# Kernel tuning notes

Measured on AMD Instinct MI355X. Metric: run time of the kernel, lower is better.

Reference implementation:

```python
import jax, jax.numpy as jnp
import numpy as np

D_STATE = 16
D_CONV = 4
DT_RANK = 8


def layer_norm(x, g, b, eps=1e-5):
    m = x.mean(-1, keepdims=True)
    v = ((x - m) ** 2).mean(-1, keepdims=True)
    return (x - m) / jnp.sqrt(v + eps) * g + b


def rms_norm(x, w, eps=1e-5):
    return x * jax.lax.rsqrt(jnp.mean(x * x, -1, keepdims=True) + eps) * w


def mamba_layer(feat, in_proj_w, conv_w, conv_b, x_proj_w, dt_proj_w, dt_proj_b,
                A_log, D_param, out_proj_w, rms_w):
    # feat: [N, C] treated as a length-N sequence with batch 1 (residual block)
    x_in = rms_norm(feat, rms_w)
    xz = x_in @ in_proj_w                         # [N, 2*d_inner]
    d_inner = conv_w.shape[0]
    x, z = xz[:, :d_inner], xz[:, d_inner:]
    # causal depthwise conv1d (torch pad=d_conv-1 then truncate to L)
    L = x.shape[0]
    x_pad = jnp.pad(x, ((D_CONV - 1, 0), (0, 0)))
    xc = conv_b + sum(x_pad[k:k + L, :] * conv_w[:, k] for k in range(D_CONV))
    x = jax.nn.silu(xc)
    dbc = x @ x_proj_w                            # [N, dt_rank + 2*d_state]
    delta = jax.nn.softplus(dbc[:, :DT_RANK] @ dt_proj_w + dt_proj_b)  # [N, d_inner]
    Bm = dbc[:, DT_RANK:DT_RANK + D_STATE]        # [N, d_state]
    Cm = dbc[:, DT_RANK + D_STATE:]               # [N, d_state]
    A = -jnp.exp(A_log)                           # [d_inner, d_state]

    def step(h, inp):
        d_t, b_t, c_t, x_t = inp
        dA = jnp.exp(d_t[:, None] * A)            # [d_inner, d_state]
        h = dA * h + d_t[:, None] * b_t[None, :] * x_t[:, None]
        y_t = (h * c_t[None, :]).sum(-1)          # [d_inner]
        return h, y_t

    h0 = jnp.zeros((d_inner, D_STATE), feat.dtype)
    _, y = jax.lax.scan(step, h0, (delta, Bm, Cm, x))
    y = y + D_param * x
    y = y * jax.nn.silu(z)
    return feat + y @ out_proj_w                  # residual


def setup_inputs() -> dict:
    N, K, C = 32768, 16, 128
    d_inner = 2 * C
    key = jax.random.key(0)
    ks = jax.random.split(key, 12)
    s = 0.02
    inp = {
        "feat": jax.random.normal(ks[0], (N, C), jnp.float32),
        "coord": jax.random.normal(ks[1], (N, 3), jnp.float32),
        "reference_index": jax.random.randint(ks[2], (N, K), 0, N, jnp.int32),
        "gauss_dist": jax.random.uniform(ks[3], (N, K), jnp.float32),
        "j": 0,
        # Mamba params
        "in_proj_w": jax.random.normal(ks[4], (C, 2 * d_inner), jnp.float32) * s,
        "conv_w": jax.random.normal(ks[5], (d_inner, D_CONV), jnp.float32) * s,
        "conv_b": jnp.zeros((d_inner,), jnp.float32),
        "x_proj_w": jax.random.normal(ks[6], (d_inner, DT_RANK + 2 * D_STATE), jnp.float32) * s,
        "dt_proj_w": jax.random.normal(ks[7], (DT_RANK, d_inner), jnp.float32) * s,
        "dt_proj_b": jax.random.uniform(ks[8], (d_inner,), jnp.float32) * 0.1,
        "A_log": jnp.log(jnp.tile(jnp.arange(1.0, D_STATE + 1.0, dtype=jnp.float32), (d_inner, 1))),
        "D_param": jnp.ones((d_inner,), jnp.float32),
        "out_proj_w": jax.random.normal(ks[9], (d_inner, C), jnp.float32) * s,
        "rms_w": jnp.ones((C,), jnp.float32),
        # PointBatchNorm (LayerNorm) shared for both norms
        "ln_g": jnp.ones((C,), jnp.float32),
        "ln_b": jnp.zeros((C,), jnp.float32),
        # linear_attention: Linear(2C->C), LayerNorm, ReLU, Linear(C->C)
        "la_w1": jax.random.normal(ks[10], (2 * C, C), jnp.float32) * s,
        "la_b1": jnp.zeros((C,), jnp.float32),
        "la_ln_g": jnp.ones((C,), jnp.float32),
        "la_ln_b": jnp.zeros((C,), jnp.float32),
        "la_w2": jax.random.normal(ks[11], (C, C), jnp.float32) * s,
        "la_b2": jnp.zeros((C,), jnp.float32),
    }
    return inp


def reference(feat, coord, reference_index, gauss_dist, j,
              in_proj_w, conv_w, conv_b, x_proj_w, dt_proj_w, dt_proj_b,
              A_log, D_param, out_proj_w, rms_w, ln_g, ln_b,
              la_w1, la_b1, la_ln_g, la_ln_b, la_w2, la_b2):
    # pointops.grouping(with_xyz=False): gather neighbor features [N, K, C]
    group_feat = feat[reference_index]
    combined = (gauss_dist[..., None] * group_feat).sum(axis=1)     # [N, C]
    combined = layer_norm(combined, ln_g, ln_b)
    feat_mamba = mamba_layer(feat, in_proj_w, conv_w, conv_b, x_proj_w,
                             dt_proj_w, dt_proj_b, A_log, D_param,
                             out_proj_w, rms_w)
    feat_mamba = layer_norm(feat_mamba, ln_g, ln_b)
    cat_feat = jnp.concatenate([feat_mamba, combined], axis=-1)     # [N, 2C]
    h = jax.nn.relu(layer_norm(cat_feat @ la_w1 + la_b1, la_ln_g, la_ln_b))
    return h @ la_w2 + la_b2
```

## Files before the change

kernel.cpp:

```cpp
#include <hip/hip_runtime.h>
#include <hip/hip_bf16.h>
#include <math.h>

#define N_TOK 32768
#define LC 32
#define NCHUNK (N_TOK / LC)
#define NSEG 64
#define SEGLEN (NCHUNK / NSEG)
#define MIDROWS 67
#define XPAD 264

typedef short short8 __attribute__((ext_vector_type(8)));
typedef float f32x4 __attribute__((ext_vector_type(4)));

__device__ __forceinline__ float siluf_(float v){ return v / (1.f + __expf(-v)); }
__device__ __forceinline__ float softplusf_(float v){ return v > 20.f ? v : log1pf(__expf(v)); }

__device__ __forceinline__ unsigned f2bfu(float f){
  __hip_bfloat16 h = __float2bfloat16(f);
  return (unsigned)*(unsigned short*)&h;
}
__device__ __forceinline__ float bfu2f(unsigned short u){
  __hip_bfloat16 h; *(unsigned short*)&h = u; return __bfloat162float(h);
}

__device__ __forceinline__ float waveRed64(float v){
  #pragma unroll
  for (int m = 1; m < 64; m <<= 1) v += __shfl_xor(v, m);
  return v;
}

__device__ __forceinline__ void pow_chain(float w, float pw[16]){
  pw[0]=w; pw[1]=w*w; pw[2]=pw[1]*w; pw[3]=pw[1]*pw[1];
  pw[4]=pw[3]*pw[0]; pw[5]=pw[3]*pw[1]; pw[6]=pw[3]*pw[2]; pw[7]=pw[3]*pw[3];
  pw[8]=pw[7]*pw[0]; pw[9]=pw[7]*pw[1]; pw[10]=pw[7]*pw[2]; pw[11]=pw[7]*pw[3];
  pw[12]=pw[7]*pw[4]; pw[13]=pw[7]*pw[5]; pw[14]=pw[7]*pw[6]; pw[15]=pw[7]*pw[7];
}

__device__ __forceinline__ bool check_intA(const float aS[16]){
  bool ok = true;
  #pragma unroll
  for (int s=0;s<16;s++){
    float tgt = (float)(s+1);
    if (fabsf(-aS[s] - tgt) > 1e-4f*tgt) ok = false;
  }
  return ok;
}

__global__ void __launch_bounds__(256) k_front(const float* __restrict__ feat,
                        const int* __restrict__ ridx,
                        const float* __restrict__ gd, const float* __restrict__ g,
                        const float* __restrict__ b, const float* __restrict__ rmsw,
                        unsigned* __restrict__ catB, unsigned* __restrict__ a0u,
                        const float* __restrict__ ipw, const float* __restrict__ opw,
                        const float* __restrict__ w1, const float* __restrict__ w2,
                        const float* __restrict__ xpw,
                        __hip_bfloat16* __restrict__ ipwt, __hip_bfloat16* __restrict__ opwt,
                        __hip_bfloat16* __restrict__ w1t, __hip_bfloat16* __restrict__ w2t,
                        __hip_bfloat16* __restrict__ xpwt){
  int bid = blockIdx.x;
  if (bid >= 8192){
    int e = (bid-8192)*256 + threadIdx.x;
    if (e < 65536){ int n=e>>7, k=e&127; ipwt[e]=__float2bfloat16(ipw[k*512+n]); }
    else if (e < 98304){ int f=e-65536; int n=f>>8, k=f&255; opwt[f]=__float2bfloat16(opw[k*128+n]); }
    else if (e < 131072){ int f=e-98304; int n=f>>8, k=f&255; w1t[f]=__float2bfloat16(w1[k*128+n]); }
    else if (e < 147456){ int f=e-131072; int n=f>>7, k=f&127; w2t[f]=__float2bfloat16(w2[k*128+n]); }
    else if (e < 159744){ int f=e-147456; int n=f>>8, k=f&255;
                          xpwt[f]=(n<40)?__float2bfloat16(xpw[k*40+n]):__float2bfloat16(0.f); }
    return;
  }
  int row = bid*4 + (threadIdx.x>>6);
  int lane = threadIdx.x & 63;
  float2 f2 = ((const float2*)feat)[row*64 + lane];
  float ss = waveRed64(f2.x*f2.x + f2.y*f2.y);
  float is0 = rsqrtf(ss * (1.f/128.f) + 1e-5f);
  float2 w = ((const float2*)rmsw)[lane];
  a0u[row*64 + lane] = f2bfu(f2.x*is0*w.x) | (f2bfu(f2.y*is0*w.y) << 16);
  float ax=0.f, ay=0.f;
  #pragma unroll 4
  for (int k=0;k<16;k++){
    int idx = ridx[row*16+k];
    float ww = gd[row*16+k];
    float2 f = ((const float2*)feat)[idx*64 + lane];
    ax += ww*f.x; ay += ww*f.y;
  }
  float m = waveRed64(ax+ay) * (1.f/128.f);
  float dx = ax-m, dy = ay-m;
  float var = waveRed64(dx*dx+dy*dy) * (1.f/128.f);
  float is = rsqrtf(var + 1e-5f);
  float2 gg = ((const float2*)g)[lane];
  float2 bb = ((const float2*)b)[lane];
  float ox = dx*is*gg.x + bb.x, oy = dy*is*gg.y + bb.y;
  catB[row*64 + lane] = f2bfu(ox) | (f2bfu(oy) << 16);
}

__global__ __launch_bounds__(256) void k_mid(
      const __hip_bfloat16* __restrict__ a0,
      const __hip_bfloat16* __restrict__ ipwt,
      const __hip_bfloat16* __restrict__ xpwt,
      const float* __restrict__ cw, const float* __restrict__ cb,
      const float* __restrict__ dtw, const float* __restrict__ dtb,
      __hip_bfloat16* __restrict__ zb,
      unsigned* __restrict__ dxb,
      float* __restrict__ Bm, float* __restrict__ Cm){
  __shared__ __align__(16) __hip_bfloat16 Xs[MIDROWS][XPAD];
  __shared__ __align__(16) float DT[64][8];
  int tid = threadIdx.x;
  int wave = tid>>6, lane = tid&63;
  int lane16 = lane&15, quad = lane>>4;
  int r0 = blockIdx.x*64;

  int n_base = wave*128;
  #pragma unroll
  for (int i=0;i<5;i++){
    int ldsbase = i*16;
    int t_lane = r0 - 3 + ldsbase + lane16;
    int tc = t_lane < 0 ? 0 : (t_lane > N_TOK-1 ? N_TOK-1 : t_lane);
    const __hip_bfloat16* Ab = a0 + (size_t)tc*128 + quad*8;
    short8 afr[4];
    #pragma unroll
    for (int k4=0;k4<4;k4++) afr[k4] = *(const short8*)(Ab + k4*32);
    #pragma unroll
    for (int j=0;j<8;j++){
      int n = n_base + j*16;
      const __hip_bfloat16* Bb = ipwt + (size_t)(n + lane16)*128 + quad*8;
      f32x4 acc = (f32x4){0.f,0.f,0.f,0.f};
      #pragma unroll
      for (int k4=0;k4<4;k4++){
        short8 bfr = *(const short8*)(Bb + k4*32);
        acc = __builtin_amdgcn_mfma_f32_16x16x32_bf16(afr[k4], bfr, acc, 0, 0, 0);
      }
      int nc = n + lane16;
      #pragma unroll
      for (int r=0;r<4;r++){
        int ldsrow = ldsbase + quad*4 + r;
        int t = r0 - 3 + ldsrow;
        float v = acc[r];
        if (nc < 256){
          if (ldsrow < MIDROWS)
            Xs[ldsrow][nc] = __float2bfloat16(t < 0 ? 0.f : v);
        } else {
          int trel = t - r0;
          if (trel >= 0 && trel < 64)
            zb[(size_t)t*256 + (nc-256)] = __float2bfloat16(siluf_(v));
        }
      }
    }
  }
  __syncthreads();

  {
    int d = tid;
    float cw0=cw[d*4], cw1=cw[d*4+1], cw2=cw[d*4+2], cw3=cw[d*4+3], cbb=cb[d];
    float a_0 = __bfloat162float(Xs[0][d]);
    float a_1 = __bfloat162float(Xs[1][d]);
    float a_2 = __bfloat162float(Xs[2][d]);
    #pragma unroll 4
    for (int t=0;t<64;t++){
      float a_3 = __bfloat162float(Xs[t+3][d]);
      float xc = siluf_(cbb + cw0*a_0 + cw1*a_1 + cw2*a_2 + cw3*a_3);
      Xs[t+3][d] = __float2bfloat16(xc);
      a_0=a_1; a_1=a_2; a_2=a_3;
    }
  }
  __syncthreads();

  {
    int m0 = wave*16;
    f32x4 acc3[3];
    #pragma unroll
    for (int j=0;j<3;j++) acc3[j] = (f32x4){0.f,0.f,0.f,0.f};
    const __hip_bfloat16* Arow = &Xs[3 + m0 + lane16][0] + quad*8;
    const __hip_bfloat16* Bb = xpwt + (size_t)lane16*256 + quad*8;
    #pragma unroll
    for (int kk=0; kk<256; kk+=32){
      short8 a  = *(const short8*)(Arow + kk);
      short8 b0 = *(const short8*)(Bb + kk);
      short8 b1 = *(const short8*)(Bb + 16*256 + kk);
      short8 b2 = *(const short8*)(Bb + 32*256 + kk);
      acc3[0] = __builtin_amdgcn_mfma_f32_16x16x32_bf16(a, b0, acc3[0], 0, 0, 0);
      acc3[1] = __builtin_amdgcn_mfma_f32_16x16x32_bf16(a, b1, acc3[1], 0, 0, 0);
      acc3[2] = __builtin_amdgcn_mfma_f32_16x16x32_bf16(a, b2, acc3[2], 0, 0, 0);
    }
    #pragma unroll
    for (int j=0;j<3;j++){
      int n = j*16 + lane16;
      #pragma unroll
      for (int r=0;r<4;r++){
        int m = m0 + quad*4 + r;
        float v = acc3[j][r];
        if (n < 8)       DT[m][n] = v;
        else if (n < 24) Bm[(size_t)(r0+m)*16 + (n-8)] = v;
        else if (n < 40) Cm[(size_t)(r0+m)*16 + (n-24)] = v;
      }
    }
  }
  __syncthreads();

  {
    int d = tid;
    float w8[8];
    #pragma unroll
    for (int j=0;j<8;j++) w8[j] = dtw[j*256+d];
    float dbias = dtb[d];
    #pragma unroll 4
    for (int t=0;t<64;t++){
      const float4* T = (const float4*)&DT[t][0];
      float4 u = T[0], v = T[1];
      float acc = dbias
        + u.x*w8[0] + u.y*w8[1] + u.z*w8[2] + u.w*w8[3]
        + v.x*w8[4] + v.y*w8[5] + v.z*w8[6] + v.w*w8[7];
      float dv = softplusf_(acc);
      unsigned xu = *(const unsigned short*)&Xs[t+3][d];
      dxb[(size_t)(r0+t)*256 + d] = f2bfu(dv) | (xu << 16);
    }
  }
}

__global__ __launch_bounds__(256) void k_scan1(const unsigned* __restrict__ dxb,
      const float* __restrict__ Bm, const float* __restrict__ A_log,
      float* __restrict__ dsum_o, __hip_bfloat16* __restrict__ Hc){
  __shared__ float Bl[LC][16];
  int g = blockIdx.x;
  int tid = threadIdx.x;
  int d = tid;
  int t0 = g*LC;
  if (tid < LC*4) ((float4*)&Bl[0][0])[tid] = ((const float4*)(Bm + (size_t)t0*16))[tid];
  __syncthreads();
  float aS[16];
  #pragma unroll
  for (int s=0;s<16;s++) aS[s] = -__expf(A_log[d*16+s]);
  bool fastA = check_intA(aS);
  float h[16] = {};
  float dsum = 0.f;
  if (fastA){
    #pragma unroll 4
    for (int t=0;t<LC;t++){
      unsigned u = dxb[(size_t)(t0+t)*256 + d];
      float dv = bfu2f((unsigned short)(u & 0xffff));
      float xv = bfu2f((unsigned short)(u >> 16));
      const float4* Bp = (const float4*)&Bl[t][0];
      float4 b0=Bp[0], b1=Bp[1], b2=Bp[2], b3=Bp[3];
      float bl[16] = {b0.x,b0.y,b0.z,b0.w, b1.x,b1.y,b1.z,b1.w,
                      b2.x,b2.y,b2.z,b2.w, b3.x,b3.y,b3.z,b3.w};
      dsum += dv;
      float dx_ = dv*xv;
      float w[16]; pow_chain(__expf(-dv), w);
      #pragma unroll
      for (int s=0;s<16;s++) h[s] = w[s]*h[s] + dx_*bl[s];
    }
  } else {
    #pragma unroll 4
    for (int t=0;t<LC;t++){
      unsigned u = dxb[(size_t)(t0+t)*256 + d];
      float dv = bfu2f((unsigned short)(u & 0xffff));
      float xv = bfu2f((unsigned short)(u >> 16));
      const float4* Bp = (const float4*)&Bl[t][0];
      float4 b0=Bp[0], b1=Bp[1], b2=Bp[2], b3=Bp[3];
      float bl[16] = {b0.x,b0.y,b0.z,b0.w, b1.x,b1.y,b1.z,b1.w,
                      b2.x,b2.y,b2.z,b2.w, b3.x,b3.y,b3.z,b3.w};
      dsum += dv;
      float dx_ = dv*xv;
      #pragma unroll
      for (int s=0;s<16;s++) h[s] = __expf(dv*aS[s])*h[s] + dx_*bl[s];
    }
  }
  dsum_o[(size_t)g*256 + d] = dsum;
  unsigned u[8];
  #pragma unroll
  for (int q=0;q<8;q++) u[q] = f2bfu(h[2*q]) | (f2bfu(h[2*q+1]) << 16);
  uint4* Hd = (uint4*)(Hc + (size_t)g*4096 + (size_t)d*16);
  Hd[0] = make_uint4(u[0],u[1],u[2],u[3]);
  Hd[1] = make_uint4(u[4],u[5],u[6],u[7]);
}

__global__ __launch_bounds__(256) void k_carry_a(const float* __restrict__ dsum,
      __hip_bfloat16* __restrict__ Hc, const float* __restrict__ A_log,
      float* __restrict__ dsum_pre, float* __restrict__ segsum, float* __restrict__ Hagg){
  int seg = blockIdx.x;
  int ch  = blockIdx.y*256 + threadIdx.x;
  int d = ch>>4, s = ch&15;
  float aSv = -__expf(A_log[ch]);
  float dpre = 0.f, c = 0.f;
  int g0 = seg*SEGLEN;
  #pragma unroll 4
  for (int i=0;i<SEGLEN;i++){
    int g = g0+i;
    float ds = dsum[(size_t)g*256 + d];
    size_t a = (size_t)g*4096 + ch;
    float hh = __bfloat162float(Hc[a]);
    float p = __expf(ds*aSv);
    if (s==0) dsum_pre[(size_t)g*256 + d] = dpre;
    Hc[a] = __float2bfloat16(c);
    dpre += ds;
    c = p*c + hh;
  }
  if (s==0) segsum[seg*256 + d] = dpre;
  Hagg[(size_t)seg*4096 + ch] = c;
}

__global__ __launch_bounds__(256) void k_carry_b(const float* __restrict__ segsum,
      const float* __restrict__ Hagg, const float* __restrict__ A_log,
      float* __restrict__ Cseg){
  int ch = blockIdx.x*256 + threadIdx.x;
  int d = ch>>4;
  float aSv = -__expf(A_log[ch]);
  float c = 0.f;
  #pragma unroll 8
  for (int s=0;s<NSEG;s++){
    Cseg[(size_t)s*4096 + ch] = c;
    c = __expf(segsum[s*256 + d]*aSv)*c + Hagg[(size_t)s*4096 + ch];
  }
}

__global__ __launch_bounds__(256) void k_scan2(const unsigned* __restrict__ dxb,
      const __hip_bfloat16* __restrict__ zb, const float* __restrict__ Bm,
      const float* __restrict__ Cm, const float* __restrict__ A_log,
      const float* __restrict__ Dp, const float* __restrict__ dsum_pre,
      const __hip_bfloat16* __restrict__ Hc, const float* __restrict__ Cseg,
      __hip_bfloat16* __restrict__ yb){
  __shared__ float Bl[LC][16];
  __shared__ float Cl[LC][16];
  int g = blockIdx.x;
  int tid = threadIdx.x;
  int d = tid;
  int t0 = g*LC;
  if (tid < 128) ((float4*)&Bl[0][0])[tid] = ((const float4*)(Bm + (size_t)t0*16))[tid];
  else ((float4*)&Cl[0][0])[tid-128] = ((const float4*)(Cm + (size_t)t0*16))[tid-128];
  __syncthreads();
  int seg = g / SEGLEN;
  float aS[16];
  #pragma unroll
  for (int s=0;s<16;s++) aS[s] = -__expf(A_log[d*16+s]);
  bool fastA = check_intA(aS);
  float h[16];
  {
    float dpre = dsum_pre[(size_t)g*256 + d];
    const uint4* hp = (const uint4*)(Hc + (size_t)g*4096 + (size_t)d*16);
    uint4 H0 = hp[0], H1 = hp[1];
    unsigned hu[8] = {H0.x,H0.y,H0.z,H0.w, H1.x,H1.y,H1.z,H1.w};
    const float4* cs = (const float4*)(Cseg + (size_t)seg*4096 + (size_t)d*16);
    float ws[16];
    if (fastA){
      pow_chain(__expf(-dpre), ws);
    } else {
      #pragma unroll
      for (int s=0;s<16;s++) ws[s] = __expf(dpre*aS[s]);
    }
    #pragma unroll
    for (int q=0;q<4;q++){
      float4 C = cs[q];
      h[q*4+0] = ws[q*4+0]*C.x + bfu2f((unsigned short)(hu[q*2]   & 0xffff));
      h[q*4+1] = ws[q*4+1]*C.y + bfu2f((unsigned short)(hu[q*2]   >> 16));
      h[q*4+2] = ws[q*4+2]*C.z + bfu2f((unsigned short)(hu[q*2+1] & 0xffff));
      h[q*4+3] = ws[q*4+3]*C.w + bfu2f((unsigned short)(hu[q*2+1] >> 16));
    }
  }
  float dpar = Dp[d];
  if (fastA){
    #pragma unroll 4
    for (int t=0;t<LC;t++){
      unsigned u = dxb[(size_t)(t0+t)*256 + d];
      float dv = bfu2f((unsigned short)(u & 0xffff));
      float xv = bfu2f((unsigned short)(u >> 16));
      float zv = __bfloat162float(zb[(size_t)(t0+t)*256 + d]);
      const float4* Bp = (const float4*)&Bl[t][0];
      const float4* Cp = (const float4*)&Cl[t][0];
      float4 b0=Bp[0], b1=Bp[1], b2=Bp[2], b3=Bp[3];
      float4 c0=Cp[0], c1=Cp[1], c2=Cp[2], c3=Cp[3];
      float bl[16] = {b0.x,b0.y,b0.z,b0.w, b1.x,b1.y,b1.z,b1.w,
                      b2.x,b2.y,b2.z,b2.w, b3.x,b3.y,b3.z,b3.w};
      float cl[16] = {c0.x,c0.y,c0.z,c0.w, c1.x,c1.y,c1.z,c1.w,
                      c2.x,c2.y,c2.z,c2.w, c3.x,c3.y,c3.z,c3.w};
      float dx_ = dv*xv;
      float w[16]; pow_chain(__expf(-dv), w);
      float yv = 0.f;
      #pragma unroll
      for (int s=0;s<16;s++){
        h[s] = w[s]*h[s] + dx_*bl[s];
        yv += h[s]*cl[s];
      }
      yb[(size_t)(t0+t)*256 + d] = __float2bfloat16((yv + dpar*xv)*zv);
    }
  } else {
    #pragma unroll 4
    for (int t=0;t<LC;t++){
      unsigned u = dxb[(size_t)(t0+t)*256 + d];
      float dv = bfu2f((unsigned short)(u & 0xffff));
      float xv = bfu2f((unsigned short)(u >> 16));
      float zv = __bfloat162float(zb[(size_t)(t0+t)*256 + d]);
      const float4* Bp = (const float4*)&Bl[t][0];
      const float4* Cp = (const float4*)&Cl[t][0];
      float4 b0=Bp[0], b1=Bp[1], b2=Bp[2], b3=Bp[3];
      float4 c0=Cp[0], c1=Cp[1], c2=Cp[2], c3=Cp[3];
      float bl[16] = {b0.x,b0.y,b0.z,b0.w, b1.x,b1.y,b1.z,b1.w,
                      b2.x,b2.y,b2.z,b2.w, b3.x,b3.y,b3.z,b3.w};
      float cl[16] = {c0.x,c0.y,c0.z,c0.w, c1.x,c1.y,c1.z,c1.w,
                      c2.x,c2.y,c2.z,c2.w, c3.x,c3.y,c3.z,c3.w};
      float dx_ = dv*xv;
      float yv = 0.f;
      #pragma unroll
      for (int s=0;s<16;s++){
        h[s] = __expf(dv*aS[s])*h[s] + dx_*bl[s];
        yv += h[s]*cl[s];
      }
      yb[(size_t)(t0+t)*256 + d] = __float2bfloat16((yv + dpar*xv)*zv);
    }
  }
}

__global__ __launch_bounds__(256) void k_tail(const __hip_bfloat16* __restrict__ yb,
      const __hip_bfloat16* __restrict__ opwt, const float* __restrict__ feat,
      const float* __restrict__ lng, const float* __restrict__ lnb,
      const unsigned* __restrict__ catB,
      const __hip_bfloat16* __restrict__ w1t, const float* __restrict__ b1,
      const float* __restrict__ lag, const float* __restrict__ lab,
      const __hip_bfloat16* __restrict__ w2t, const float* __restrict__ b2,
      float* __restrict__ out){
  __shared__ __align__(16) float Ls[64][132];
  __shared__ __align__(16) unsigned Cu[64][132];
  int tid = threadIdx.x;
  int wave = tid>>6, lane = tid&63;
  int wm = wave>>1, wn = wave&1;
  int lane16 = lane&15, quad = lane>>4;
  int r0 = blockIdx.x*64;

  #pragma unroll
  for (int i=0;i<16;i++){
    int idx = i*256 + tid;
    int row = idx>>6, c = idx&63;
    Cu[row][64+c] = catB[(size_t)(r0+row)*64 + c];
  }

  f32x4 acc[2][4];
  #pragma unroll
  for (int i=0;i<2;i++)
    #pragma unroll
    for (int j=0;j<4;j++) acc[i][j] = (f32x4){0.f,0.f,0.f,0.f};
  {
    const __hip_bfloat16* Ab = yb   + (size_t)(r0 + wm*32 + lane16)*256 + quad*8;
    const __hip_bfloat16* Bb = opwt + (size_t)(wn*64 + lane16)*256 + quad*8;
    #pragma unroll 2
    for (int kk=0; kk<256; kk+=32){
      short8 a[2], bf[4];
      #pragma unroll
      for (int i=0;i<2;i++) a[i] = *(const short8*)(Ab + (size_t)i*16*256 + kk);
      #pragma unroll
      for (int j=0;j<4;j++) bf[j] = *(const short8*)(Bb + (size_t)j*16*256 + kk);
      #pragma unroll
      for (int i=0;i<2;i++)
        #pragma unroll
        for (int j=0;j<4;j++)
          acc[i][j] = __builtin_amdgcn_mfma_f32_16x16x32_bf16(a[i], bf[j], acc[i][j], 0, 0, 0);
    }
  }
  #pragma unroll
  for (int i=0;i<2;i++)
    #pragma unroll
    for (int j=0;j<4;j++){
      int n = wn*64 + j*16 + lane16;
      #pragma unroll
      for (int r=0;r<4;r++){
        int m = wm*32 + i*16 + quad*4 + r;
        Ls[m][n] = acc[i][j][r] + feat[(size_t)(r0+m)*128 + n];
      }
    }
  __syncthreads();
  {
    float2 gv = ((const float2*)lng)[lane];
    float2 bv = ((const float2*)lnb)[lane];
    #pragma unroll 4
    for (int rr=0; rr<16; rr++){
      int row = wave*16 + rr;
      float2 v = *(const float2*)&Ls[row][2*lane];
      float mm = waveRed64(v.x+v.y) * (1.f/128.f);
      float dx = v.x-mm, dy = v.y-mm;
      float var = waveRed64(dx*dx+dy*dy) * (1.f/128.f);
      float is = rsqrtf(var + 1e-5f);
      Cu[row][lane] = f2bfu(dx*is*gv.x + bv.x) | (f2bfu(dy*is*gv.y + bv.y) << 16);
    }
  }
  __syncthreads();
  #pragma unroll
  for (int i=0;i<2;i++)
    #pragma unroll
    for (int j=0;j<4;j++) acc[i][j] = (f32x4){0.f,0.f,0.f,0.f};
  {
    const __hip_bfloat16* Bb = w1t + (size_t)(wn*64 + lane16)*256 + quad*8;
    #pragma unroll 2
    for (int kk=0; kk<256; kk+=32){
      short8 a[2], bf[4];
      #pragma unroll
      for (int i=0;i<2;i++)
        a[i] = *(const short8*)(&Cu[wm*32 + i*16 + lane16][0] + (kk>>1) + quad*4);
      #pragma unroll
      for (int j=0;j<4;j++) bf[j] = *(const short8*)(Bb + (size_t)j*16*256 + kk);
      #pragma unroll
      for (int i=0;i<2;i++)
        #pragma unroll
        for (int j=0;j<4;j++)
          acc[i][j] = __builtin_amdgcn_mfma_f32_16x16x32_bf16(a[i], bf[j], acc[i][j], 0, 0, 0);
    }
  }
  #pragma unroll
  for (int i=0;i<2;i++)
    #pragma unroll
    for (int j=0;j<4;j++){
      int n = wn*64 + j*16 + lane16;
      float bv1 = b1[n];
      #pragma unroll
      for (int r=0;r<4;r++){
        int m = wm*32 + i*16 + quad*4 + r;
        Ls[m][n] = acc[i][j][r] + bv1;
      }
    }
  __syncthreads();
  {
    float2 gv = ((const float2*)lag)[lane];
    float2 bv = ((const float2*)lab)[lane];
    #pragma unroll 4
    for (int rr=0; rr<16; rr++){
      int row = wave*16 + rr;
      float2 v = *(const float2*)&Ls[row][2*lane];
      float mm = waveRed64(v.x+v.y) * (1.f/128.f);
      float dx = v.x-mm, dy = v.y-mm;
      float var = waveRed64(dx*dx+dy*dy) * (1.f/128.f);
      float is = rsqrtf(var + 1e-5f);
      float ox = fmaxf(dx*is*gv.x + bv.x, 0.f);
      float oy = fmaxf(dy*is*gv.y + bv.y, 0.f);
      Cu[row][lane] = f2bfu(ox) | (f2bfu(oy) << 16);
    }
  }
  __syncthreads();
  #pragma unroll
  for (int i=0;i<2;i++)
    #pragma unroll
    for (int j=0;j<4;j++) acc[i][j] = (f32x4){0.f,0.f,0.f,0.f};
  {
    const __hip_bfloat16* Bb = w2t + (size_t)(wn*64 + lane16)*128 + quad*8;
    #pragma unroll
    for (int kk=0; kk<128; kk+=32){
      short8 a[2], bf[4];
      #pragma unroll
      for (int i=0;i<2;i++)
        a[i] = *(const short8*)(&Cu[wm*32 + i*16 + lane16][0] + (kk>>1) + quad*4);
      #pragma unroll
      for (int j=0;j<4;j++) bf[j] = *(const short8*)(Bb + (size_t)j*16*128 + kk);
      #pragma unroll
      for (int i=0;i<2;i++)
        #pragma unroll
        for (int j=0;j<4;j++)
          acc[i][j] = __builtin_amdgcn_mfma_f32_16x16x32_bf16(a[i], bf[j], acc[i][j], 0, 0, 0);
    }
  }
  #pragma unroll
  for (int i=0;i<2;i++)
    #pragma unroll
    for (int j=0;j<4;j++){
      int n = wn*64 + j*16 + lane16;
      float bv2 = b2[n];
      #pragma unroll
      for (int r=0;r<4;r++){
        int m = wm*32 + i*16 + quad*4 + r;
        out[(size_t)(r0+m)*128 + n] = acc[i][j][r] + bv2;
      }
    }
}

extern "C" void kernel_launch(void* const* d_in, const int* in_sizes, int n_in,
                              void* d_out, int out_size, void* d_ws, size_t ws_size,
                              hipStream_t stream){
  const float* feat = (const float*)d_in[0];
  const int*   ridx = (const int*)d_in[2];
  const float* gd   = (const float*)d_in[3];
  const float* ipw  = (const float*)d_in[5];
  const float* cw   = (const float*)d_in[6];
  const float* cb   = (const float*)d_in[7];
  const float* xpw  = (const float*)d_in[8];
  const float* dtw  = (const float*)d_in[9];
  const float* dtb  = (const float*)d_in[10];
  const float* alog = (const float*)d_in[11];
  const float* dpar = (const float*)d_in[12];
  const float* opw  = (const float*)d_in[13];
  const float* rmsw = (const float*)d_in[14];
  const float* lng  = (const float*)d_in[15];
  const float* lnb  = (const float*)d_in[16];
  const float* w1   = (const float*)d_in[17];
  const float* b1   = (const float*)d_in[18];
  const float* lag  = (const float*)d_in[19];
  const float* lab  = (const float*)d_in[20];
  const float* w2   = (const float*)d_in[21];
  const float* b2   = (const float*)d_in[22];
  float* out = (float*)d_out;

  char* p = (char*)d_ws;
  __hip_bfloat16* zb   = (__hip_bfloat16*)p; p += (size_t)N_TOK*256*2;
  unsigned* dxb        = (unsigned*)p;       p += (size_t)N_TOK*256*4;
  unsigned* catB       = (unsigned*)p;       p += (size_t)N_TOK*64*4;
  __hip_bfloat16* yb   = (__hip_bfloat16*)p; p += (size_t)N_TOK*256*2;
  float* Bm   = (float*)p; p += (size_t)N_TOK*16*4;
  float* Cm   = (float*)p; p += (size_t)N_TOK*16*4;
  __hip_bfloat16* Hc = (__hip_bfloat16*)p; p += (size_t)NCHUNK*4096*2;
  float* dsum = (float*)p; p += (size_t)NCHUNK*256*4;
  float* dpre = (float*)p; p += (size_t)NCHUNK*256*4;
  float* segs = (float*)p; p += (size_t)NSEG*256*4;
  float* Hagg = (float*)p; p += (size_t)NSEG*4096*4;
  float* Cseg = (float*)p; p += (size_t)NSEG*4096*4;
  __hip_bfloat16* ipwt = (__hip_bfloat16*)p; p += 512*128*2;
  __hip_bfloat16* opwt = (__hip_bfloat16*)p; p += 128*256*2;
  __hip_bfloat16* w1t  = (__hip_bfloat16*)p; p += 128*256*2;
  __hip_bfloat16* w2t  = (__hip_bfloat16*)p; p += 128*128*2;
  __hip_bfloat16* xpwt = (__hip_bfloat16*)p; p += 48*256*2;
  __hip_bfloat16* a0 = yb;

  hipLaunchKernelGGL(k_front, dim3(8192+624), dim3(256), 0, stream,
                     feat, ridx, gd, lng, lnb, rmsw, catB, (unsigned*)a0,
                     ipw, opw, w1, w2, xpw, ipwt, opwt, w1t, w2t, xpwt);
  hipLaunchKernelGGL(k_mid, dim3(N_TOK/64), dim3(256), 0, stream,
                     a0, ipwt, xpwt, cw, cb, dtw, dtb, zb, dxb, Bm, Cm);
  hipLaunchKernelGGL(k_scan1, dim3(NCHUNK), dim3(256), 0, stream,
                     dxb, Bm, alog, dsum, Hc);
  hipLaunchKernelGGL(k_carry_a, dim3(NSEG, 16), dim3(256), 0, stream,
                     dsum, Hc, alog, dpre, segs, Hagg);
  hipLaunchKernelGGL(k_carry_b, dim3(16), dim3(256), 0, stream, segs, Hagg, alog, Cseg);
  hipLaunchKernelGGL(k_scan2, dim3(NCHUNK), dim3(256), 0, stream,
                     dxb, zb, Bm, Cm, alog, dpar, dpre, Hc, Cseg, yb);
  hipLaunchKernelGGL(k_tail, dim3(N_TOK/64), dim3(256), 0, stream,
                     yb, opwt, feat, lng, lnb, catB, w1t, b1, lag, lab, w2t, b2, out);
}
```

Before: 305.5 us.

## Split fused in_proj/conv kernel into a tiled MFMA GEMM and a conv/x_proj kernel

Replaces the fused k_mid kernel, which recomputed in_proj for three halo rows per 64-token block and reloaded weight fragments per tile. A separate register-tiled 4x4 MFMA GEMM now writes the x half to a new bf16 buffer and silu(z) to zb. A new k_cxd kernel handles 32 tokens per block, loading x rows plus halo from that buffer into LDS for the causal conv, x_proj and delta. The split adds an extra N×256 bf16 global round-trip and one more launch, in exchange for better GEMM reuse and more blocks in the conv stage.

After: 305.1 us. No clear change (-0.1%).

```diff
diff --git a/kernel.cpp b/kernel.cpp
--- a/kernel.cpp
+++ b/kernel.cpp
@@ -7,7 +7,8 @@
 #define NCHUNK (N_TOK / LC)
 #define NSEG 64
 #define SEGLEN (NCHUNK / NSEG)
-#define MIDROWS 67
+#define CXT 32
+#define CXROWS 35
 #define XPAD 264
 
 typedef short short8 __attribute__((ext_vector_type(8)));
@@ -94,58 +95,73 @@
   catB[row*64 + lane] = f2bfu(ox) | (f2bfu(oy) << 16);
 }
 
-__global__ __launch_bounds__(256) void k_mid(
-      const __hip_bfloat16* __restrict__ a0,
-      const __hip_bfloat16* __restrict__ ipwt,
+template<int WM16, int WN16>
+__global__ __launch_bounds__(256) void k_mfma(const __hip_bfloat16* __restrict__ A,
+      const __hip_bfloat16* __restrict__ Wt, int K,
+      __hip_bfloat16* __restrict__ out0b, __hip_bfloat16* __restrict__ out1){
+  int tid = threadIdx.x;
+  int wave = tid>>6, lane = tid&63;
+  int wm = wave>>1, wn = wave&1;
+  int lane16 = lane&15, quad = lane>>4;
+  int m_w = blockIdx.x*(2*WM16*16) + wm*(WM16*16);
+  int n_w = blockIdx.y*(2*WN16*16) + wn*(WN16*16);
+  f32x4 acc[WM16][WN16];
+  #pragma unroll
+  for (int i=0;i<WM16;i++)
+    #pragma unroll
+    for (int j=0;j<WN16;j++) acc[i][j] = (f32x4){0.f,0.f,0.f,0.f};
+  const __hip_bfloat16* Ab = A  + (size_t)(m_w + lane16)*K + quad*8;
+  const __hip_bfloat16* Bb = Wt + (size_t)(n_w + lane16)*K + quad*8;
+  #pragma unroll 4
+  for (int kk=0; kk<K; kk+=32){
+    short8 a[WM16], b[WN16];
+    #pragma unroll
+    for (int i=0;i<WM16;i++) a[i] = *(const short8*)(Ab + (size_t)i*16*K + kk);
+    #pragma unroll
+    for (int j=0;j<WN16;j++) b[j] = *(const short8*)(Bb + (size_t)j*16*K + kk);
+    #pragma unroll
+    for (int i=0;i<WM16;i++)
+      #pragma unroll
+      for (int j=0;j<WN16;j++)
+        acc[i][j] = __builtin_amdgcn_mfma_f32_16x16x32_bf16(a[i], b[j], acc[i][j], 0, 0, 0);
+  }
+  #pragma unroll
+  for (int i=0;i<WM16;i++){
+    #pragma unroll
+    for (int j=0;j<WN16;j++){
+      int n = n_w + j*16 + lane16;
+      #pragma unroll
+      for (int r=0;r<4;r++){
+        int m = m_w + i*16 + quad*4 + r;
+        float v = acc[i][j][r];
+        if (n < 256) out0b[(size_t)m*256 + n] = __float2bfloat16(v);
+        else         out1[(size_t)m*256 + (n-256)] = __float2bfloat16(siluf_(v));
+      }
+    }
+  }
+}
+
+__global__ __launch_bounds__(256) void k_cxd(
+      const __hip_bfloat16* __restrict__ bxb,
       const __hip_bfloat16* __restrict__ xpwt,
       const float* __restrict__ cw, const float* __restrict__ cb,
       const float* __restrict__ dtw, const float* __restrict__ dtb,
-      __hip_bfloat16* __restrict__ zb,
       unsigned* __restrict__ dxb,
       float* __restrict__ Bm, float* __restrict__ Cm){
-  __shared__ __align__(16) __hip_bfloat16 Xs[MIDROWS][XPAD];
-  __shared__ __align__(16) float DT[64][8];
+  __shared__ __align__(16) __hip_bfloat16 Xs[CXROWS][XPAD];
+  __shared__ __align__(16) float DT[CXT][8];
   int tid = threadIdx.x;
   int wave = tid>>6, lane = tid&63;
   int lane16 = lane&15, quad = lane>>4;
-  int r0 = blockIdx.x*64;
-
-  int n_base = wave*128;
-  #pragma unroll
-  for (int i=0;i<5;i++){
-    int ldsbase = i*16;
-    int t_lane = r0 - 3 + ldsbase + lane16;
-    int tc = t_lane < 0 ? 0 : (t_lane > N_TOK-1 ? N_TOK-1 : t_lane);
-    const __hip_bfloat16* Ab = a0 + (size_t)tc*128 + quad*8;
-    short8 afr[4];
-    #pragma unroll
-    for (int k4=0;k4<4;k4++) afr[k4] = *(const short8*)(Ab + k4*32);
-    #pragma unroll
-    for (int j=0;j<8;j++){
-      int n = n_base + j*16;
-      const __hip_bfloat16* Bb = ipwt + (size_t)(n + lane16)*128 + quad*8;
-      f32x4 acc = (f32x4){0.f,0.f,0.f,0.f};
-      #pragma unroll
-      for (int k4=0;k4<4;k4++){
-        short8 bfr = *(const short8*)(Bb + k4*32);
-        acc = __builtin_amdgcn_mfma_f32_16x16x32_bf16(afr[k4], bfr, acc, 0, 0, 0);
-      }
-      int nc = n + lane16;
-      #pragma unroll
-      for (int r=0;r<4;r++){
-        int ldsrow = ldsbase + quad*4 + r;
-        int t = r0 - 3 + ldsrow;
-        float v = acc[r];
-        if (nc < 256){
-          if (ldsrow < MIDROWS)
-            Xs[ldsrow][nc] = __float2bfloat16(t < 0 ? 0.f : v);
-        } else {
-          int trel = t - r0;
-          if (trel >= 0 && trel < 64)
-            zb[(size_t)t*256 + (nc-256)] = __float2bfloat16(siluf_(v));
-        }
-      }
-    }
+  int r0 = blockIdx.x*CXT;
+
+  #pragma unroll
+  for (int idx = tid; idx < CXROWS*32; idx += 256){
+    int row = idx>>5, col = idx&31;
+    int t = r0 - 3 + row;
+    uint4 v = (t >= 0) ? ((const uint4*)(bxb + (size_t)t*256))[col]
+                       : make_uint4(0,0,0,0);
+    ((uint4*)&Xs[row][0])[col] = v;
   }
   __syncthreads();
 
@@ -156,7 +172,7 @@
     float a_1 = __bfloat162float(Xs[1][d]);
     float a_2 = __bfloat162float(Xs[2][d]);
     #pragma unroll 4
-    for (int t=0;t<64;t++){
+    for (int t=0;t<CXT;t++){
       float a_3 = __bfloat162float(Xs[t+3][d]);
       float xc = siluf_(cbb + cw0*a_0 + cw1*a_1 + cw2*a_2 + cw3*a_3);
       Xs[t+3][d] = __float2bfloat16(xc);
@@ -165,7 +181,7 @@
   }
   __syncthreads();
 
-  {
+  if (wave < 2){
     int m0 = wave*16;
     f32x4 acc3[3];
     #pragma unroll
@@ -204,7 +220,7 @@
     for (int j=0;j<8;j++) w8[j] = dtw[j*256+d];
     float dbias = dtb[d];
     #pragma unroll 4
-    for (int t=0;t<64;t++){
+    for (int t=0;t<CXT;t++){
       const float4* T = (const float4*)&DT[t][0];
       float4 u = T[0], v = T[1];
       float acc = dbias
@@ -594,6 +610,7 @@
   float* out = (float*)d_out;
 
   char* p = (char*)d_ws;
+  __hip_bfloat16* bxb  = (__hip_bfloat16*)p; p += (size_t)N_TOK*256*2;
   __hip_bfloat16* zb   = (__hip_bfloat16*)p; p += (size_t)N_TOK*256*2;
   unsigned* dxb        = (unsigned*)p;       p += (size_t)N_TOK*256*4;
   unsigned* catB       = (unsigned*)p;       p += (size_t)N_TOK*64*4;
@@ -616,8 +633,10 @@
   hipLaunchKernelGGL(k_front, dim3(8192+624), dim3(256), 0, stream,
                      feat, ridx, gd, lng, lnb, rmsw, catB, (unsigned*)a0,
                      ipw, opw, w1, w2, xpw, ipwt, opwt, w1t, w2t, xpwt);
-  hipLaunchKernelGGL(k_mid, dim3(N_TOK/64), dim3(256), 0, stream,
-                     a0, ipwt, xpwt, cw, cb, dtw, dtb, zb, dxb, Bm, Cm);
+  hipLaunchKernelGGL((k_mfma<4,4>), dim3(N_TOK/128, 4), dim3(256), 0, stream,
+                     a0, ipwt, 128, bxb, zb);
+  hipLaunchKernelGGL(k_cxd, dim3(N_TOK/CXT), dim3(256), 0, stream,
+                     bxb, xpwt, cw, cb, dtw, dtb, dxb, Bm, Cm);
   hipLaunchKernelGGL(k_scan1, dim3(NCHUNK), dim3(256), 0, stream,
                      dxb, Bm, alog, dsum, Hc);
   hipLaunchKernelGGL(k_carry_a, dim3(NSEG, 16), dim3(256), 0, stream,
```
